# Kernel optimization log

Measured on AMD Instinct MI355X. Metric: run time of the kernel, lower is better.

The kernel has to match this reference:

```python
import math
import jax, jax.numpy as jnp
import numpy as np

B, LA, LB, H = 16, 1024, 1024, 512
NEG = -10000000.0


def setup_inputs() -> dict:
    key = jax.random.key(0)
    k1, k2, k3, k4 = jax.random.split(key, 4)
    a = jax.random.normal(k1, (B, LA, H), dtype=jnp.float32)
    b = jax.random.normal(k2, (B, LB, H), dtype=jnp.float32)
    mask_a = jax.random.randint(k3, (B, LA, 1), 0, 2, dtype=jnp.int32)
    mask_b = jax.random.randint(k4, (B, LB, 1), 0, 2, dtype=jnp.int32)
    temperature = jnp.asarray(1.0 / math.sqrt(H), dtype=jnp.float32)
    return {"a": a, "b": b, "mask_a": mask_a, "mask_b": mask_b, "temperature": temperature}


def reference(a, b, mask_a, mask_b, temperature):
    # attn[b,i,j] = <a_i, b_j> * temperature  -> [B, LA, LB]
    attn = jnp.einsum("bid,bjd->bij", a, b) * temperature
    # pairwise validity mask: outer product of per-token masks
    mask = jnp.einsum("bik,bjk->bij", mask_a.astype(jnp.float32), mask_b.astype(jnp.float32)) > 0
    attn = jnp.where(mask, attn, NEG)
    attn_a = jax.nn.softmax(attn, axis=1)  # softmax over a-tokens
    attn_b = jax.nn.softmax(attn, axis=2)  # softmax over b-tokens
    feature_b = jnp.einsum("bij,bid->bjd", attn_a, a)  # [B, LB, H]
    feature_a = jnp.einsum("bij,bjd->bid", attn_b, b)  # [B, LA, H]
    return (feature_a, feature_b)
```

## Files before the change

### kernel.cpp

```cpp
#include <hip/hip_runtime.h>
#include <hip/hip_bf16.h>

#define NB_ 16
#define LA_ 1024
#define LB_ 1024
#define H_  512

typedef __attribute__((ext_vector_type(8))) short short8;
typedef __attribute__((ext_vector_type(4))) float f32x4;

using bf16 = __hip_bfloat16;

__device__ __forceinline__ float bf2f(unsigned short u) {
    union { unsigned int i; float f; } c; c.i = ((unsigned)u) << 16; return c.f;
}
__device__ __forceinline__ unsigned short f2bf(float f) {
    bf16 h = __float2bfloat16(f);
    return *(unsigned short*)&h;
}

__device__ __forceinline__ void load_lds16(const void* g, void* l) {
    __builtin_amdgcn_global_load_lds(
        (const __attribute__((address_space(1))) void*)g,
        (__attribute__((address_space(3))) void*)l, 16, 0, 0);
}

__device__ __forceinline__ void gemm_core64(
    const unsigned short* __restrict__ A, const unsigned short* __restrict__ B,
    int lda, int ldb, int K,
    unsigned short* ldsA, unsigned short* ldsB, f32x4 acc[4][4])
{
    const int t = threadIdx.x;
    const int wave = t >> 6, lane = t & 63;
    const int wr = wave >> 1, wc = wave & 1;
    const int lm = lane & 15, q = lane >> 4;

    int aoff[4], boff[4];
#pragma unroll
    for (int f = 0; f < 4; f++) {
        const int ra = wr * 64 + f * 16 + lm;
        aoff[f] = ra * 128 + ((q ^ (ra & 7)) << 4);
        const int rb = wc * 64 + f * 16 + lm;
        boff[f] = rb * 128 + ((q ^ (rb & 7)) << 4);
    }

    const int row0 = wave * 8 + (lane >> 3);
    const int sc = (lane & 7) ^ (row0 & 7);
    const unsigned short* gA0 = A + (size_t)row0 * lda + sc * 8;
    const unsigned short* gB0 = B + (size_t)row0 * ldb + sc * 8;
    const int sA = 32 * lda, sB = 32 * ldb;
    char* lA = (char*)ldsA + wave * 1024;
    char* lB = (char*)ldsB + wave * 1024;

    for (int k0 = 0; k0 < K; k0 += 64) {
        __syncthreads();
#pragma unroll
        for (int s = 0; s < 4; s++) {
            load_lds16(gA0 + k0 + s * sA, lA + s * 4096);
            load_lds16(gB0 + k0 + s * sB, lB + s * 4096);
        }
        __syncthreads();
#pragma unroll
        for (int kk = 0; kk < 2; kk++) {
            const int kx = kk << 6;
            short8 av[4];
#pragma unroll
            for (int fm = 0; fm < 4; fm++)
                av[fm] = *(const short8*)((const char*)ldsA + (aoff[fm] ^ kx));
#pragma unroll
            for (int fn = 0; fn < 4; fn++) {
                const short8 bv = *(const short8*)((const char*)ldsB + (boff[fn] ^ kx));
#pragma unroll
                for (int fm = 0; fm < 4; fm++)
                    acc[fm][fn] = __builtin_amdgcn_mfma_f32_16x16x32_bf16(
                        av[fm], bv, acc[fm][fn], 0, 0, 0);
            }
        }
    }
}

__global__ __launch_bounds__(256) void k_gemm_attn(
    const unsigned short* __restrict__ a_bf, const unsigned short* __restrict__ b_bf,
    const int* __restrict__ mask_a, const int* __restrict__ mask_b,
    const float* __restrict__ temp_p,
    unsigned short* __restrict__ E, unsigned short* __restrict__ ET,
    float* __restrict__ l_row, float* __restrict__ l_col)
{
    __shared__ unsigned short lds[16384];
    unsigned short* ldsA = lds;
    unsigned short* ldsB = lds + 8192;

    const int batch = blockIdx.z;
    const int i0 = blockIdx.y * 128, j0 = blockIdx.x * 128;
    const unsigned short* A = a_bf + (size_t)batch * LA_ * H_ + (size_t)i0 * H_;
    const unsigned short* B = b_bf + (size_t)batch * LB_ * H_ + (size_t)j0 * H_;
    f32x4 acc[4][4];
#pragma unroll
    for (int x = 0; x < 4; x++)
#pragma unroll
        for (int y = 0; y < 4; y++) acc[x][y] = 0;

    gemm_core64(A, B, H_, H_, H_, ldsA, ldsB, acc);

    const float temp = temp_p[0];
    const int t = threadIdx.x, wave = t >> 6, lane = t & 63;
    const int wr = wave >> 1, wc = wave & 1, lm = lane & 15, q = lane >> 4;
    const int* map = mask_a + batch * LA_;
    const int* mbp = mask_b + batch * LB_;
    unsigned short* Ep  = E  + (size_t)batch * LA_ * LB_;
    unsigned short* ETp = ET + (size_t)batch * LB_ * LA_;
    float* lrp = l_row + batch * LA_;
    float* lcp = l_col + batch * LB_;

    int mb[4];
#pragma unroll
    for (int fn = 0; fn < 4; fn++) mb[fn] = mbp[j0 + wc * 64 + fn * 16 + lm];

#pragma unroll
    for (int fm = 0; fm < 4; fm++) {
        const int ib = i0 + wr * 64 + fm * 16 + q * 4;
        int ma[4];
#pragma unroll
        for (int r = 0; r < 4; r++) ma[r] = map[ib + r];
#pragma unroll
        for (int fn = 0; fn < 4; fn++) {
            const int j = j0 + wc * 64 + fn * 16 + lm;
            ushort4 pk;
            unsigned short* pp = (unsigned short*)&pk;
#pragma unroll
            for (int r = 0; r < 4; r++) {
                const float e = (ma[r] && mb[fn]) ? __expf(acc[fm][fn][r] * temp) : 0.0f;
                acc[fm][fn][r] = e;
                pp[r] = f2bf(e);
            }
            *(ushort4*)(ETp + (size_t)j * LA_ + ib) = pk;
        }
    }

#pragma unroll
    for (int fm = 0; fm < 4; fm++)
#pragma unroll
        for (int r = 0; r < 4; r++) {
            float s = acc[fm][0][r] + acc[fm][1][r] + acc[fm][2][r] + acc[fm][3][r];
            s += __shfl_xor(s, 1, 16); s += __shfl_xor(s, 2, 16);
            s += __shfl_xor(s, 4, 16); s += __shfl_xor(s, 8, 16);
            if (lm == 0) atomicAdd(&lrp[i0 + wr * 64 + fm * 16 + q * 4 + r], s);
        }
#pragma unroll
    for (int fn = 0; fn < 4; fn++) {
        float s = 0.0f;
#pragma unroll
        for (int fm = 0; fm < 4; fm++)
#pragma unroll
            for (int r = 0; r < 4; r++) s += acc[fm][fn][r];
        s += __shfl_xor(s, 16, 64); s += __shfl_xor(s, 32, 64);
        if (lane < 16) atomicAdd(&lcp[j0 + wc * 64 + fn * 16 + lm], s);
    }

    __syncthreads();
#pragma unroll
    for (int fm = 0; fm < 4; fm++)
#pragma unroll
        for (int fn = 0; fn < 4; fn++)
#pragma unroll
            for (int r = 0; r < 4; r++) {
                const int il = wr * 64 + fm * 16 + q * 4 + r;
                const int jl = wc * 64 + fn * 16 + lm;
                lds[il * 128 + (((jl >> 3) ^ ((il >> 1) & 7)) << 3) + (jl & 7)] =
                    f2bf(acc[fm][fn][r]);
            }
    __syncthreads();
#pragma unroll
    for (int rep = 0; rep < 8; rep++) {
        const int il = (t >> 4) + rep * 16;
        const int jc = t & 15;
        const int phys = jc ^ ((il >> 1) & 7);
        short8 v = *(const short8*)(lds + il * 128 + phys * 8);
        *(short8*)(Ep + (size_t)(i0 + il) * LB_ + j0 + jc * 8) = v;
    }
}

__global__ __launch_bounds__(256) void k_gemm_feat(
    const unsigned short* __restrict__ E, const unsigned short* __restrict__ ET,
    const unsigned short* __restrict__ aT, const unsigned short* __restrict__ bT,
    const int* __restrict__ mask_a, const int* __restrict__ mask_b,
    const int* __restrict__ nA, const int* __restrict__ nB,
    const float* __restrict__ l_row, const float* __restrict__ l_col,
    const float* __restrict__ mean_a, const float* __restrict__ mean_b,
    float* __restrict__ out)
{
    __shared__ unsigned short lds[16384];
    unsigned short* ldsA = lds;
    unsigned short* ldsB = lds + 8192;

    const int z = blockIdx.z;
    const int batch = z & 15;
    const bool isA = z < 16;
    const unsigned short* Amat = (isA ? E : ET) + (size_t)batch * 1024 * 1024;
    const unsigned short* Bm   = (isA ? bT : aT) + (size_t)batch * H_ * 1024;
    const int* mp   = (isA ? mask_a : mask_b) + batch * 1024;
    const int nn    = (isA ? nB : nA)[batch];
    const float* sp = (isA ? l_row : l_col) + batch * 1024;
    const float* mv = (isA ? mean_b : mean_a) + batch * H_;
    float* op = out + (isA ? (size_t)0 : (size_t)NB_ * LA_ * H_) + (size_t)batch * 1024 * H_;

    const int m0 = blockIdx.y * 128, n0 = blockIdx.x * 128;
    f32x4 acc[4][4];
#pragma unroll
    for (int x = 0; x < 4; x++)
#pragma unroll
        for (int y = 0; y < 4; y++) acc[x][y] = 0;

    gemm_core64(Amat + (size_t)m0 * 1024, Bm + (size_t)n0 * 1024,
                1024, 1024, 1024, ldsA, ldsB, acc);

    const int t = threadIdx.x, wave = t >> 6, lane = t & 63;
    const int wr = wave >> 1, wc = wave & 1, lm = lane & 15, q = lane >> 4;

    float mval[4];
#pragma unroll
    for (int fn = 0; fn < 4; fn++) mval[fn] = mv[n0 + wc * 64 + fn * 16 + lm];

#pragma unroll
    for (int fm = 0; fm < 4; fm++) {
        const int ib = m0 + wr * 64 + fm * 16 + q * 4;
#pragma unroll
        for (int r = 0; r < 4; r++) {
            const int i = ib + r;
            const bool valid = (mp[i] != 0) && (nn > 0);
            const float inv = valid ? 1.0f / sp[i] : 0.0f;
#pragma unroll
            for (int fn = 0; fn < 4; fn++) {
                const int d = n0 + wc * 64 + fn * 16 + lm;
                op[(size_t)i * H_ + d] = valid ? acc[fm][fn][r] * inv : mval[fn];
            }
        }
    }
}

__global__ __launch_bounds__(256) void k_prep(
    const float* __restrict__ a, const float* __restrict__ b,
    unsigned short* __restrict__ aN, unsigned short* __restrict__ bN,
    unsigned short* __restrict__ aT, unsigned short* __restrict__ bT,
    float* __restrict__ mean_a, float* __restrict__ mean_b)
{
    __shared__ unsigned short lds[64][68];
    __shared__ float smean[64];
    const int z = blockIdx.z;
    const int batch = z & 15, sel = z >> 4;
    const float* src = sel ? b : a;
    unsigned short* np = (sel ? bN : aN) + (size_t)batch * 1024 * H_;
    unsigned short* tp = (sel ? bT : aT) + (size_t)batch * H_ * 1024;
    float* mdst = (sel ? mean_b : mean_a) + batch * H_;
    const float* sp = src + (size_t)batch * 1024 * H_;

    const int d0 = blockIdx.x * 64, i0 = blockIdx.y * 64;
    const int t = threadIdx.x;
    if (t < 64) smean[t] = 0.0f;
    const int c4 = (t & 15) * 4;
#pragma unroll
    for (int it = 0; it < 4; it++) {
        const int r = (t >> 4) + it * 16;
        float4 v = *(const float4*)(sp + (size_t)(i0 + r) * H_ + d0 + c4);
        ushort4 u = make_ushort4(f2bf(v.x), f2bf(v.y), f2bf(v.z), f2bf(v.w));
        *(ushort4*)(np + (size_t)(i0 + r) * H_ + d0 + c4) = u;
        *(ushort4*)&lds[r][c4] = u;
    }
    __syncthreads();
#pragma unroll
    for (int it = 0; it < 4; it++) {
        const int dd = (t >> 4) + it * 16;
        const int i4 = (t & 15) * 4;
        ushort4 u = make_ushort4(lds[i4][dd], lds[i4 + 1][dd], lds[i4 + 2][dd], lds[i4 + 3][dd]);
        *(ushort4*)(tp + (size_t)(d0 + dd) * 1024 + i0 + i4) = u;
        atomicAdd(&smean[dd], bf2f(u.x) + bf2f(u.y) + bf2f(u.z) + bf2f(u.w));
    }
    __syncthreads();
    if (t < 64) atomicAdd(&mdst[d0 + t], smean[t] * (1.0f / 1024.0f));
}

__global__ __launch_bounds__(256) void k_count(const int* __restrict__ mask_a,
                                               const int* __restrict__ mask_b,
                                               int* __restrict__ nA, int* __restrict__ nB)
{
    const int batch = blockIdx.x, t = threadIdx.x;
    int sa = 0, sb = 0;
    for (int i = t; i < 1024; i += 256) {
        sa += mask_a[batch * 1024 + i];
        sb += mask_b[batch * 1024 + i];
    }
    __shared__ int ra[256], rb[256];
    ra[t] = sa; rb[t] = sb;
    __syncthreads();
    for (int off = 128; off; off >>= 1) {
        if (t < off) { ra[t] += ra[t + off]; rb[t] += rb[t + off]; }
        __syncthreads();
    }
    if (t == 0) { nA[batch] = ra[0]; nB[batch] = rb[0]; }
}

extern "C" void kernel_launch(void* const* d_in, const int* in_sizes, int n_in,
                              void* d_out, int out_size, void* d_ws, size_t ws_size,
                              hipStream_t stream)
{
    const float* a      = (const float*)d_in[0];
    const float* b      = (const float*)d_in[1];
    const int*   mask_a = (const int*)d_in[2];
    const int*   mask_b = (const int*)d_in[3];
    const float* temp   = (const float*)d_in[4];
    float* out = (float*)d_out;

    char* ws = (char*)d_ws;
    size_t off = 0;
    unsigned short* E    = (unsigned short*)(ws + off); off += (size_t)NB_ * LA_ * LB_ * 2;
    unsigned short* ET   = (unsigned short*)(ws + off); off += (size_t)NB_ * LB_ * LA_ * 2;
    unsigned short* a_bf = (unsigned short*)(ws + off); off += (size_t)NB_ * LA_ * H_ * 2;
    unsigned short* b_bf = (unsigned short*)(ws + off); off += (size_t)NB_ * LB_ * H_ * 2;
    unsigned short* aT   = (unsigned short*)(ws + off); off += (size_t)NB_ * H_ * LA_ * 2;
    unsigned short* bT   = (unsigned short*)(ws + off); off += (size_t)NB_ * H_ * LB_ * 2;
    float* l_row  = (float*)(ws + off); off += (size_t)NB_ * LA_ * 4;
    float* l_col  = (float*)(ws + off); off += (size_t)NB_ * LB_ * 4;
    float* mean_a = (float*)(ws + off); off += (size_t)NB_ * H_ * 4;
    float* mean_b = (float*)(ws + off); off += (size_t)NB_ * H_ * 4;
    int*   nA     = (int*)(ws + off); off += 64;
    int*   nB     = (int*)(ws + off); off += 64;

    hipMemsetAsync(l_row, 0, (size_t)NB_ * (LA_ + LB_ + H_ + H_) * 4, stream);

    k_prep<<<dim3(H_ / 64, 1024 / 64, 32), 256, 0, stream>>>(
        a, b, a_bf, b_bf, aT, bT, mean_a, mean_b);
    k_count<<<dim3(NB_), 256, 0, stream>>>(mask_a, mask_b, nA, nB);

    k_gemm_attn<<<dim3(LB_ / 128, LA_ / 128, NB_), 256, 0, stream>>>(
        a_bf, b_bf, mask_a, mask_b, temp, E, ET, l_row, l_col);

    k_gemm_feat<<<dim3(H_ / 128, 1024 / 128, 32), 256, 0, stream>>>(
        E, ET, aT, bT, mask_a, mask_b, nA, nB, l_row, l_col, mean_a, mean_b, out);
}
```

Measured before the change: 245.6 us.

## Double-buffer LDS with K-step 32 and prefetch the next tile during MFMA

The shared GEMM core now uses a K-step of 32 instead of 64 and splits the existing 32KB LDS into two ping-pong buffers. Global-to-LDS loads for the next K-slice are issued before computing on the current one, with a single barrier per iteration. The aim is to overlap memory traffic with MFMA work instead of stalling at each load barrier. In exchange the loop runs twice as many iterations, and a new swizzle pattern is needed for the narrower rows.

New measurement: 256.7 us. 4.5% more time.

```diff
diff --git a/kernel.cpp b/kernel.cpp
--- a/kernel.cpp
+++ b/kernel.cpp
@@ -25,10 +25,10 @@
         (__attribute__((address_space(3))) void*)l, 16, 0, 0);
 }
 
-__device__ __forceinline__ void gemm_core64(
+__device__ __forceinline__ void gemm_core32(
     const unsigned short* __restrict__ A, const unsigned short* __restrict__ B,
     int lda, int ldb, int K,
-    unsigned short* ldsA, unsigned short* ldsB, f32x4 acc[4][4])
+    unsigned short* lds, f32x4 acc[4][4])
 {
     const int t = threadIdx.x;
     const int wave = t >> 6, lane = t & 63;
@@ -39,43 +39,49 @@
 #pragma unroll
     for (int f = 0; f < 4; f++) {
         const int ra = wr * 64 + f * 16 + lm;
-        aoff[f] = ra * 128 + ((q ^ (ra & 7)) << 4);
+        aoff[f] = ra * 64 + ((q ^ ((ra >> 1) & 3)) << 4);
         const int rb = wc * 64 + f * 16 + lm;
-        boff[f] = rb * 128 + ((q ^ (rb & 7)) << 4);
-    }
-
-    const int row0 = wave * 8 + (lane >> 3);
-    const int sc = (lane & 7) ^ (row0 & 7);
-    const unsigned short* gA0 = A + (size_t)row0 * lda + sc * 8;
-    const unsigned short* gB0 = B + (size_t)row0 * ldb + sc * 8;
-    const int sA = 32 * lda, sB = 32 * ldb;
-    char* lA = (char*)ldsA + wave * 1024;
-    char* lB = (char*)ldsB + wave * 1024;
-
-    for (int k0 = 0; k0 < K; k0 += 64) {
+        boff[f] = rb * 64 + ((q ^ ((rb >> 1) & 3)) << 4) + 8192;
+    }
+
+    const int r4 = lane >> 2, pc = lane & 3;
+    const int srcc = pc ^ ((r4 >> 1) & 3);
+    const unsigned short* gA0 = A + (size_t)(wave * 32 + r4) * lda + srcc * 8;
+    const unsigned short* gA1 = gA0 + 16 * lda;
+    const unsigned short* gB0 = B + (size_t)(wave * 32 + r4) * ldb + srcc * 8;
+    const unsigned short* gB1 = gB0 + 16 * ldb;
+    char* lwA = (char*)lds + wave * 2048;
+    char* lwB = (char*)lds + 8192 + wave * 2048;
+
+    load_lds16(gA0, lwA);
+    load_lds16(gA1, lwA + 1024);
+    load_lds16(gB0, lwB);
+    load_lds16(gB1, lwB + 1024);
+
+    int bo = 0;
+    for (int k0 = 0; k0 < K; k0 += 32) {
         __syncthreads();
-#pragma unroll
-        for (int s = 0; s < 4; s++) {
-            load_lds16(gA0 + k0 + s * sA, lA + s * 4096);
-            load_lds16(gB0 + k0 + s * sB, lB + s * 4096);
-        }
-        __syncthreads();
-#pragma unroll
-        for (int kk = 0; kk < 2; kk++) {
-            const int kx = kk << 6;
-            short8 av[4];
+        if (k0 + 32 < K) {
+            const int nb = bo ^ 16384;
+            load_lds16(gA0 + k0 + 32, lwA + nb);
+            load_lds16(gA1 + k0 + 32, lwA + nb + 1024);
+            load_lds16(gB0 + k0 + 32, lwB + nb);
+            load_lds16(gB1 + k0 + 32, lwB + nb + 1024);
+        }
+        const char* base = (const char*)lds + bo;
+        short8 av[4];
+#pragma unroll
+        for (int fm = 0; fm < 4; fm++)
+            av[fm] = *(const short8*)(base + aoff[fm]);
+#pragma unroll
+        for (int fn = 0; fn < 4; fn++) {
+            const short8 bv = *(const short8*)(base + boff[fn]);
 #pragma unroll
             for (int fm = 0; fm < 4; fm++)
-                av[fm] = *(const short8*)((const char*)ldsA + (aoff[fm] ^ kx));
-#pragma unroll
-            for (int fn = 0; fn < 4; fn++) {
-                const short8 bv = *(const short8*)((const char*)ldsB + (boff[fn] ^ kx));
-#pragma unroll
-                for (int fm = 0; fm < 4; fm++)
-                    acc[fm][fn] = __builtin_amdgcn_mfma_f32_16x16x32_bf16(
-                        av[fm], bv, acc[fm][fn], 0, 0, 0);
-            }
-        }
+                acc[fm][fn] = __builtin_amdgcn_mfma_f32_16x16x32_bf16(
+                    av[fm], bv, acc[fm][fn], 0, 0, 0);
+        }
+        bo ^= 16384;
     }
 }
 
@@ -87,8 +93,6 @@
     float* __restrict__ l_row, float* __restrict__ l_col)
 {
     __shared__ unsigned short lds[16384];
-    unsigned short* ldsA = lds;
-    unsigned short* ldsB = lds + 8192;
 
     const int batch = blockIdx.z;
     const int i0 = blockIdx.y * 128, j0 = blockIdx.x * 128;
@@ -100,7 +104,7 @@
 #pragma unroll
         for (int y = 0; y < 4; y++) acc[x][y] = 0;
 
-    gemm_core64(A, B, H_, H_, H_, ldsA, ldsB, acc);
+    gemm_core32(A, B, H_, H_, H_, lds, acc);
 
     const float temp = temp_p[0];
     const int t = threadIdx.x, wave = t >> 6, lane = t & 63;
@@ -190,8 +194,6 @@
     float* __restrict__ out)
 {
     __shared__ unsigned short lds[16384];
-    unsigned short* ldsA = lds;
-    unsigned short* ldsB = lds + 8192;
 
     const int z = blockIdx.z;
     const int batch = z & 15;
@@ -211,8 +213,8 @@
 #pragma unroll
         for (int y = 0; y < 4; y++) acc[x][y] = 0;
 
-    gemm_core64(Amat + (size_t)m0 * 1024, Bm + (size_t)n0 * 1024,
-                1024, 1024, 1024, ldsA, ldsB, acc);
+    gemm_core32(Amat + (size_t)m0 * 1024, Bm + (size_t)n0 * 1024,
+                1024, 1024, 1024, lds, acc);
 
     const int t = threadIdx.x, wave = t >> 6, lane = t & 63;
     const int wr = wave >> 1, wc = wave & 1, lm = lane & 15, q = lane >> 4;
```

## Fuse memset and mask counting into one init kernel; remap GEMM grids batch-fastest

Applied to the files above, without the earlier changes.

Replaces the hipMemsetAsync plus the separate mask-count kernel with a single k_init launch that zeroes the accumulators and counts masks per batch in parallel blocks. Both GEMM kernels move to a flattened 1D grid where batch (and A/B side) is the fastest-varying index. Co-scheduled blocks then come from different batches, which changes L2/MALL locality and how work spreads across XCDs. The cost removed is one launch/memset, and the remap is a locality gamble.

Measured after the change: 227.3 us. 7.5% less time.

```diff
diff --git a/kernel.cpp b/kernel.cpp
--- a/kernel.cpp
+++ b/kernel.cpp
@@ -90,8 +90,11 @@
     unsigned short* ldsA = lds;
     unsigned short* ldsB = lds + 8192;
 
-    const int batch = blockIdx.z;
-    const int i0 = blockIdx.y * 128, j0 = blockIdx.x * 128;
+    const int g = blockIdx.x;
+    const int batch = g & 15;
+    const int qq = g >> 4;
+    const int i0 = (qq >> 3) * 128, j0 = (qq & 7) * 128;
+
     const unsigned short* A = a_bf + (size_t)batch * LA_ * H_ + (size_t)i0 * H_;
     const unsigned short* B = b_bf + (size_t)batch * LB_ * H_ + (size_t)j0 * H_;
     f32x4 acc[4][4];
@@ -193,9 +196,13 @@
     unsigned short* ldsA = lds;
     unsigned short* ldsB = lds + 8192;
 
-    const int z = blockIdx.z;
-    const int batch = z & 15;
-    const bool isA = z < 16;
+    const int g = blockIdx.x;
+    const int zc = g & 31;
+    const int qq = g >> 5;
+    const int n0 = (qq & 3) * 128, m0 = (qq >> 2) * 128;
+
+    const int batch = zc & 15;
+    const bool isA = zc < 16;
     const unsigned short* Amat = (isA ? E : ET) + (size_t)batch * 1024 * 1024;
     const unsigned short* Bm   = (isA ? bT : aT) + (size_t)batch * H_ * 1024;
     const int* mp   = (isA ? mask_a : mask_b) + batch * 1024;
@@ -204,7 +211,6 @@
     const float* mv = (isA ? mean_b : mean_a) + batch * H_;
     float* op = out + (isA ? (size_t)0 : (size_t)NB_ * LA_ * H_) + (size_t)batch * 1024 * H_;
 
-    const int m0 = blockIdx.y * 128, n0 = blockIdx.x * 128;
     f32x4 acc[4][4];
 #pragma unroll
     for (int x = 0; x < 4; x++)
@@ -279,24 +285,28 @@
     if (t < 64) atomicAdd(&mdst[d0 + t], smean[t] * (1.0f / 1024.0f));
 }
 
-__global__ __launch_bounds__(256) void k_count(const int* __restrict__ mask_a,
-                                               const int* __restrict__ mask_b,
-                                               int* __restrict__ nA, int* __restrict__ nB)
-{
-    const int batch = blockIdx.x, t = threadIdx.x;
-    int sa = 0, sb = 0;
-    for (int i = t; i < 1024; i += 256) {
-        sa += mask_a[batch * 1024 + i];
-        sb += mask_b[batch * 1024 + i];
-    }
-    __shared__ int ra[256], rb[256];
-    ra[t] = sa; rb[t] = sb;
+__global__ __launch_bounds__(256) void k_init(
+    float* __restrict__ accum_zero,
+    const int* __restrict__ mask_a, const int* __restrict__ mask_b,
+    int* __restrict__ nA, int* __restrict__ nB)
+{
+    const int g = blockIdx.x, t = threadIdx.x;
+    if (g < 48) {
+        *(float4*)(accum_zero + (size_t)(g * 256 + t) * 4) = make_float4(0, 0, 0, 0);
+        return;
+    }
+    const int sel = g - 48;
+    const int batch = sel & 15, which = sel >> 4;
+    const int* m = (which ? mask_b : mask_a) + batch * 1024;
+    int s = m[t] + m[t + 256] + m[t + 512] + m[t + 768];
+    __shared__ int red[256];
+    red[t] = s;
     __syncthreads();
     for (int off = 128; off; off >>= 1) {
-        if (t < off) { ra[t] += ra[t + off]; rb[t] += rb[t + off]; }
+        if (t < off) red[t] += red[t + off];
         __syncthreads();
     }
-    if (t == 0) { nA[batch] = ra[0]; nB[batch] = rb[0]; }
+    if (t == 0) (which ? nB : nA)[batch] = red[0];
 }
 
 extern "C" void kernel_launch(void* const* d_in, const int* in_sizes, int n_in,
@@ -325,15 +335,14 @@
     int*   nA     = (int*)(ws + off); off += 64;
     int*   nB     = (int*)(ws + off); off += 64;
 
-    hipMemsetAsync(l_row, 0, (size_t)NB_ * (LA_ + LB_ + H_ + H_) * 4, stream);
+    k_init<<<dim3(80), 256, 0, stream>>>(l_row, mask_a, mask_b, nA, nB);
 
     k_prep<<<dim3(H_ / 64, 1024 / 64, 32), 256, 0, stream>>>(
         a, b, a_bf, b_bf, aT, bT, mean_a, mean_b);
-    k_count<<<dim3(NB_), 256, 0, stream>>>(mask_a, mask_b, nA, nB);
-
-    k_gemm_attn<<<dim3(LB_ / 128, LA_ / 128, NB_), 256, 0, stream>>>(
+
+    k_gemm_attn<<<dim3(1024), 256, 0, stream>>>(
         a_bf, b_bf, mask_a, mask_b, temp, E, ET, l_row, l_col);
 
-    k_gemm_feat<<<dim3(H_ / 128, 1024 / 128, 32), 256, 0, stream>>>(
+    k_gemm_feat<<<dim3(1024), 256, 0, stream>>>(
         E, ET, aT, bT, mask_a, mask_b, nA, nB, l_row, l_col, mean_a, mean_b, out);
 }
```
